# Optimization experiments

Hardware: AMD Instinct MI355X
Metric: run time of the kernel (lower is better)

## Reference

```python
import jax, jax.numpy as jnp
import numpy as np

N_NODES = 100000
N_EDGES = 1600000
IN_DIM, HIDDEN, OUT_DIM = 128, 64, 32
LN_EPS = 1e-5


def setup_inputs() -> dict:
    key = jax.random.key(0)
    ks = jax.random.split(key, 12)
    x = jax.random.normal(ks[0], (N_NODES, IN_DIM), dtype=jnp.float32)
    edge_index = jax.random.randint(ks[1], (2, N_EDGES), 0, N_NODES, dtype=jnp.int64)
    s = 1.0 / np.sqrt(IN_DIM)
    s2 = 1.0 / np.sqrt(HIDDEN)
    return {
        "x": x,
        "edge_index": edge_index,
        "W_self0": jax.random.uniform(ks[2], (IN_DIM, HIDDEN), jnp.float32, -s, s),
        "W_neigh0": jax.random.uniform(ks[3], (IN_DIM, HIDDEN), jnp.float32, -s, s),
        "b0": jnp.zeros((HIDDEN,), jnp.float32),
        "g0": jnp.ones((HIDDEN,), jnp.float32),
        "be0": jnp.zeros((HIDDEN,), jnp.float32),
        "W_self1": jax.random.uniform(ks[4], (HIDDEN, OUT_DIM), jnp.float32, -s2, s2),
        "W_neigh1": jax.random.uniform(ks[5], (HIDDEN, OUT_DIM), jnp.float32, -s2, s2),
        "b1": jnp.zeros((OUT_DIM,), jnp.float32),
        "g1": jnp.ones((OUT_DIM,), jnp.float32),
        "be1": jnp.zeros((OUT_DIM,), jnp.float32),
    }


def _sage_layer(h, src, dst, W_self, W_neigh, b, g, be):
    n = h.shape[0]
    # mean aggregation of neighbor features via scatter-add + count
    agg = jax.ops.segment_sum(h[src], dst, num_segments=n)  # [N, F]
    cnt = jax.ops.segment_sum(jnp.ones((src.shape[0],), h.dtype), dst, num_segments=n)
    agg = agg / jnp.clip(cnt, 1.0)[:, None]
    z = h @ W_self + agg @ W_neigh + b  # [N, out]
    mu = jnp.mean(z, axis=-1, keepdims=True)
    var = jnp.mean((z - mu) ** 2, axis=-1, keepdims=True)
    zn = (z - mu) * jax.lax.rsqrt(var + LN_EPS) * g + be
    return jax.nn.relu(zn)


def reference(x, edge_index, W_self0, W_neigh0, b0, g0, be0,
              W_self1, W_neigh1, b1, g1, be1):
    src, dst = edge_index[0], edge_index[1]
    h = _sage_layer(x, src, dst, W_self0, W_neigh0, b0, g0, be0)
    h = _sage_layer(h, src, dst, W_self1, W_neigh1, b1, g1, be1)
    return h
```

## Files before the change

### kernel.cpp

```cpp
#include <hip/hip_runtime.h>
#include <hip/hip_bf16.h>

#define N_NODES 100000
#define N_EDGES 1600000
#define IN_DIM 128
#define HID 64
#define OUT_DIM 32
#define LN_EPS 1e-5f
#define NBKT 782
#define NPBLK 500
#define PAIRS_PER_BLK 1600
#define G0T 1563
#define PADCAP 384

typedef __attribute__((ext_vector_type(8))) _Float16 half8;
typedef __attribute__((ext_vector_type(4))) float f32x4;

__device__ __forceinline__ float uflo(unsigned int u) {
  return __uint_as_float(u << 16);
}
__device__ __forceinline__ float ufhi(unsigned int u) {
  return __uint_as_float(u & 0xffff0000u);
}
__device__ __forceinline__ unsigned short bf16rne(float f) {
  unsigned int u = __float_as_uint(f);
  unsigned int r = u + 0x7fffu + ((u >> 16) & 1u);
  return (unsigned short)(r >> 16);
}

__global__ void detect_edges(const int* __restrict__ w, int* __restrict__ flag) {
  __shared__ int any;
  if (threadIdx.x == 0) any = 0;
  __syncthreads();
  if (w[2 * threadIdx.x + 1] != 0) any = 1;
  __syncthreads();
  if (threadIdx.x == 0) flag[0] = any ? 0 : 1;
}

__global__ __launch_bounds__(256) void convW(
    const float* __restrict__ Wn0, const float* __restrict__ Ws0,
    const float* __restrict__ Wn1, const float* __restrict__ Ws1,
    _Float16* __restrict__ B0f, _Float16* __restrict__ B1f) {
  const int i = blockIdx.x * 256 + threadIdx.x;
  if (i < 128 * 128) {
    const int n = i >> 7, k = i & 127;
    const float w = (n < 64) ? Wn0[k * 64 + n] : Ws0[k * 64 + (n - 64)];
    B0f[i] = (_Float16)w;
  } else if (i < 128 * 128 + 64 * 64) {
    const int j = i - 128 * 128;
    const int n = j >> 6, k = j & 63;
    const float w = (n < 32) ? Wn1[k * 32 + n] : Ws1[k * 32 + (n - 32)];
    B1f[j] = (_Float16)w;
  }
}

__global__ __launch_bounds__(256) void g0pc(
    const float* __restrict__ x, const _Float16* __restrict__ B0f,
    const float* __restrict__ b0,
    unsigned short* __restrict__ p0u, float* __restrict__ s0b,
    const int* __restrict__ w, const int* __restrict__ flag,
    int* __restrict__ gcount, int* __restrict__ blkbase) {
  __shared__ _Float16 lb[64 * 128];
  const int tid = threadIdx.x;

  if (blockIdx.x < NPBLK) {
    int* h = (int*)lb;
    const int b = blockIdx.x;
    for (int i = tid; i < NBKT; i += 256) h[i] = 0;
    __syncthreads();
    const int i64 = flag[0];
    const int pEnd = (b + 1) * PAIRS_PER_BLK;
    for (int p = b * PAIRS_PER_BLK + tid; p < pEnd; p += 256) {
      int d0, d1;
      if (i64) {
        const int4 vd = *(const int4*)(w + 2 * (size_t)N_EDGES + 4 * (size_t)p);
        d0 = vd.x; d1 = vd.z;
      } else {
        const int2 vd = *(const int2*)(w + (size_t)N_EDGES + 2 * (size_t)p);
        d0 = vd.x; d1 = vd.y;
      }
      atomicAdd(&h[d0 >> 7], 1);
      atomicAdd(&h[d1 >> 7], 1);
    }
    __syncthreads();
    for (int i = tid; i < NBKT; i += 256)
      blkbase[b * NBKT + i] = atomicAdd(&gcount[i], h[i]);
    return;
  }

  const int gb = blockIdx.x - NPBLK;
  const int colgrp = (gb >= G0T) ? 1 : 0;
  const int rowblk = colgrp ? (gb - G0T) : gb;
  {
    const uint4* gsrc = (const uint4*)(B0f + (colgrp << 13));
    for (int i = tid; i < 1024; i += 256) {
      const int o = i << 4;
      const int sw = o ^ (((o >> 8) & 7) << 4);
      *(uint4*)((char*)lb + sw) = gsrc[i];
    }
  }
  __syncthreads();
  const int lane = tid & 63;
  const int wave = tid >> 6;
  const int rowbase = rowblk * 64 + wave * 16;
  const int arow = rowbase + (lane & 15);
  const int rclamp = (arow < N_NODES) ? arow : 0;
  const int ko = (lane >> 4) << 3;

  f32x4 acc[4];
#pragma unroll
  for (int ct = 0; ct < 4; ++ct) acc[ct] = (f32x4){0.f, 0.f, 0.f, 0.f};

  for (int ks = 0; ks < 4; ++ks) {
    float av[8];
    const float* ax = x + (size_t)rclamp * IN_DIM + ks * 32 + ko;
    *(float4*)&av[0] = *(const float4*)ax;
    *(float4*)&av[4] = *(const float4*)(ax + 4);
    half8 ah;
#pragma unroll
    for (int j = 0; j < 8; ++j) ah[j] = (_Float16)av[j];
    const int kb = ks * 64 + (ko << 1);
#pragma unroll
    for (int ct = 0; ct < 4; ++ct) {
      const int n = ct * 16 + (lane & 15);
      const int boff = (n << 8) + kb;
      const int sb = boff ^ (((boff >> 8) & 7) << 4);
      const half8 bv = *(const half8*)((const char*)lb + sb);
      acc[ct] = __builtin_amdgcn_mfma_f32_16x16x32_f16(ah, bv, acc[ct], 0, 0, 0);
    }
  }
  const int rb4 = rowbase + ((lane >> 4) << 2);
  const int cc = lane & 15;
  if (colgrp == 0) {
#pragma unroll
    for (int ct = 0; ct < 4; ++ct) {
#pragma unroll
      for (int j = 0; j < 4; ++j) {
        const int r = rb4 + j;
        if (r < N_NODES) p0u[(size_t)r * HID + ct * 16 + cc] = bf16rne(acc[ct][j]);
      }
    }
  } else {
#pragma unroll
    for (int ct = 0; ct < 4; ++ct) {
      const float bias = b0[ct * 16 + cc];
#pragma unroll
      for (int j = 0; j < 4; ++j) {
        const int r = rb4 + j;
        if (r < N_NODES) s0b[(size_t)r * HID + ct * 16 + cc] = acc[ct][j] + bias;
      }
    }
  }
}

__global__ __launch_bounds__(256) void part_scan(
    const int* __restrict__ gcount, int* __restrict__ gbase) {
  __shared__ int lds[256];
  const int t = threadIdx.x;
  int v[4];
  int s = 0;
#pragma unroll
  for (int j = 0; j < 4; ++j) {
    const int idx = t * 4 + j;
    v[j] = (idx < NBKT) ? gcount[idx] : 0;
    s += v[j];
  }
  lds[t] = s;
  __syncthreads();
  for (int o = 1; o < 256; o <<= 1) {
    const int val = (t >= o) ? lds[t - o] : 0;
    __syncthreads();
    lds[t] += val;
    __syncthreads();
  }
  int run = lds[t] - s;
#pragma unroll
  for (int j = 0; j < 4; ++j) {
    const int idx = t * 4 + j;
    if (idx < NBKT) gbase[idx] = run;
    run += v[j];
  }
}

__global__ __launch_bounds__(256) void part_scatter(
    const int* __restrict__ w, const int* __restrict__ flag,
    const int* __restrict__ gbase, const int* __restrict__ blkbase,
    int* __restrict__ pe) {
  __shared__ int cur[NBKT];
  const int t = threadIdx.x, b = blockIdx.x;
  for (int i = t; i < NBKT; i += 256)
    cur[i] = gbase[i] + blkbase[b * NBKT + i];
  __syncthreads();
  const int i64 = flag[0];
  const int pEnd = (b + 1) * PAIRS_PER_BLK;
  for (int p = b * PAIRS_PER_BLK + t; p < pEnd; p += 256) {
    int s0, s1, d0, d1;
    if (i64) {
      const int4 vs = *(const int4*)(w + 4 * (size_t)p);
      const int4 vd = *(const int4*)(w + 2 * (size_t)N_EDGES + 4 * (size_t)p);
      s0 = vs.x; s1 = vs.z;
      d0 = vd.x; d1 = vd.z;
    } else {
      const int2 vs = *(const int2*)(w + 2 * (size_t)p);
      const int2 vd = *(const int2*)(w + (size_t)N_EDGES + 2 * (size_t)p);
      s0 = vs.x; s1 = vs.y;
      d0 = vd.x; d1 = vd.y;
    }
    const int sl0 = atomicAdd(&cur[d0 >> 7], 1);
    pe[sl0] = s0 | ((d0 & 127) << 17);
    const int sl1 = atomicAdd(&cur[d1 >> 7], 1);
    pe[sl1] = s1 | ((d1 & 127) << 17);
  }
}

__global__ __launch_bounds__(256) void bucket_csr(
    const int* __restrict__ pe, const int* __restrict__ gbase,
    const int* __restrict__ gcount, int* __restrict__ deg,
    int* __restrict__ off, int* __restrict__ sortedSrc) {
  __shared__ int ldeg[128];
  __shared__ int loff[128];
  __shared__ int lcur[128];
  const int t = threadIdx.x;
  const int bkt = blockIdx.x;
  const int nbase = bkt << 7;
  const int ebase = gbase[bkt];
  const int cnt = gcount[bkt];
  const int outbase = ebase + PADCAP * bkt;
  if (t < 128) ldeg[t] = 0;
  __syncthreads();
  for (int e = t; e < cnt; e += 256) {
    const int pv = pe[ebase + e];
    atomicAdd(&ldeg[(pv >> 17) & 127], 1);
  }
  __syncthreads();
  if (t < 128) loff[t] = (ldeg[t] + 3) & ~3;
  __syncthreads();
  for (int o = 1; o < 128; o <<= 1) {
    int v = 0;
    if (t >= o && t < 128) v = loff[t - o];
    __syncthreads();
    if (t < 128) loff[t] += v;
    __syncthreads();
  }
  if (t < 128) {
    const int pdeg = (ldeg[t] + 3) & ~3;
    const int ex = loff[t] - pdeg;
    lcur[t] = ex;
    const int n = nbase + t;
    if (n < N_NODES) {
      deg[n] = ldeg[t];
      off[n] = outbase + ex;
    }
  }
  __syncthreads();
  for (int e = t; e < cnt; e += 256) {
    const int pv = pe[ebase + e];
    const int ld = (pv >> 17) & 127;
    const int p = atomicAdd(&lcur[ld], 1);
    sortedSrc[outbase + p] = pv & 0x1FFFF;
  }
  __syncthreads();
  if (t < 128) {
    const int pdeg = (ldeg[t] + 3) & ~3;
    const int ex = loff[t] - pdeg;
    for (int q = ldeg[t]; q < pdeg; ++q)
      sortedSrc[outbase + ex + q] = N_NODES;
  }
}

__global__ __launch_bounds__(256) void gemm1(
    const float* __restrict__ h1, const _Float16* __restrict__ B1f,
    const float* __restrict__ b1,
    unsigned short* __restrict__ p1u, float* __restrict__ s1b) {
  __shared__ _Float16 lb[64 * 64];
  const int tid = threadIdx.x;
  {
    const uint4* gb = (const uint4*)B1f;
    for (int i = tid; i < 512; i += 256) {
      const int o = i << 4;
      const int sw = o ^ (((o >> 7) & 7) << 4);
      *(uint4*)((char*)lb + sw) = gb[i];
    }
  }
  __syncthreads();
  const int lane = tid & 63;
  const int wave = tid >> 6;
  const int rowbase = blockIdx.x * 64 + wave * 16;
  const int arow = rowbase + (lane & 15);
  const int rclamp = (arow < N_NODES) ? arow : 0;
  const int ko = (lane >> 4) << 3;

  f32x4 acc[4];
#pragma unroll
  for (int ct = 0; ct < 4; ++ct) acc[ct] = (f32x4){0.f, 0.f, 0.f, 0.f};

  for (int ks = 0; ks < 2; ++ks) {
    float av[8];
    const float* ax = h1 + (size_t)rclamp * HID + ks * 32 + ko;
    *(float4*)&av[0] = *(const float4*)ax;
    *(float4*)&av[4] = *(const float4*)(ax + 4);
    half8 ah;
#pragma unroll
    for (int j = 0; j < 8; ++j) ah[j] = (_Float16)av[j];
    const int kb = ks * 64 + (ko << 1);
#pragma unroll
    for (int ct = 0; ct < 4; ++ct) {
      const int n = ct * 16 + (lane & 15);
      const int boff = (n << 7) + kb;
      const int sb = boff ^ (((boff >> 7) & 7) << 4);
      const half8 bv = *(const half8*)((const char*)lb + sb);
      acc[ct] = __builtin_amdgcn_mfma_f32_16x16x32_f16(ah, bv, acc[ct], 0, 0, 0);
    }
  }
  const int rb4 = rowbase + ((lane >> 4) << 2);
  const int cc = lane & 15;
#pragma unroll
  for (int ct = 0; ct < 2; ++ct) {
#pragma unroll
    for (int j = 0; j < 4; ++j) {
      const int r = rb4 + j;
      if (r < N_NODES) p1u[(size_t)r * OUT_DIM + ct * 16 + cc] = bf16rne(acc[ct][j]);
    }
  }
#pragma unroll
  for (int ct = 2; ct < 4; ++ct) {
    const float bias = b1[(ct - 2) * 16 + cc];
#pragma unroll
    for (int j = 0; j < 4; ++j) {
      const int r = rb4 + j;
      if (r < N_NODES)
        s1b[(size_t)r * OUT_DIM + (ct - 2) * 16 + cc] = acc[ct][j] + bias;
    }
  }
}

__global__ __launch_bounds__(256) void aggc0(
    const int* __restrict__ sortedSrc, const int* __restrict__ off,
    const int* __restrict__ deg, const unsigned short* __restrict__ p0u,
    const float* __restrict__ s0b, const float* __restrict__ g,
    const float* __restrict__ be, float* __restrict__ h1) {
  const int lane = threadIdx.x & 63;
  const int h = lane >> 5;
  const int grp = (lane >> 3) & 3;
  const int sl = lane & 7;
  const int i = blockIdx.x * 8 + ((threadIdx.x >> 6) << 1) + h;
  const int st = off[i];
  const int dg = deg[i];
  const int dgp = (dg + 3) & ~3;
  const int dgmaxp = max(dgp, __shfl_xor(dgp, 32));
  float acc[8];
#pragma unroll
  for (int f = 0; f < 8; ++f) acc[f] = 0.f;

  for (int base = 0; base < dgmaxp; base += 32) {
    const int cntp = dgp - base;
    const int l5 = lane & 31;
    const int idx = (l5 < cntp) ? sortedSrc[st + base + l5] : N_NODES;
    const int cm = min(32, dgmaxp - base);
    for (int j = 0; j * 4 < cm; ++j) {
      const int e = j * 4 + grp;
      const int srcn = __shfl(idx, (h << 5) | e);
      const uint4 q = *(const uint4*)(p0u + (size_t)srcn * HID + sl * 8);
      acc[0] += uflo(q.x); acc[1] += ufhi(q.x);
      acc[2] += uflo(q.y); acc[3] += ufhi(q.y);
      acc[4] += uflo(q.z); acc[5] += ufhi(q.z);
      acc[6] += uflo(q.w); acc[7] += ufhi(q.w);
    }
  }
#pragma unroll
  for (int mk = 8; mk < 32; mk <<= 1) {
#pragma unroll
    for (int f = 0; f < 8; ++f) acc[f] += __shfl_xor(acc[f], mk);
  }
  const float inv = 1.0f / fmaxf((float)dg, 1.0f);
  float z[8];
  const float4 sb0 = *(const float4*)(s0b + (size_t)i * HID + sl * 8);
  const float4 sb1 = *(const float4*)(s0b + (size_t)i * HID + sl * 8 + 4);
  z[0] = sb0.x + acc[0] * inv; z[1] = sb0.y + acc[1] * inv;
  z[2] = sb0.z + acc[2] * inv; z[3] = sb0.w + acc[3] * inv;
  z[4] = sb1.x + acc[4] * inv; z[5] = sb1.y + acc[5] * inv;
  z[6] = sb1.z + acc[6] * inv; z[7] = sb1.w + acc[7] * inv;
  float pm = 0.f;
#pragma unroll
  for (int f = 0; f < 8; ++f) pm += z[f];
#pragma unroll
  for (int mk = 1; mk < 8; mk <<= 1) pm += __shfl_xor(pm, mk);
  const float mean = pm * (1.0f / 64.0f);
  float pv = 0.f;
#pragma unroll
  for (int f = 0; f < 8; ++f) {
    z[f] -= mean;
    pv += z[f] * z[f];
  }
#pragma unroll
  for (int mk = 1; mk < 8; mk <<= 1) pv += __shfl_xor(pv, mk);
  const float rstd = rsqrtf(pv * (1.0f / 64.0f) + LN_EPS);
  if (grp == 0) {
    const float4 gv0 = *(const float4*)(g + sl * 8);
    const float4 gv1 = *(const float4*)(g + sl * 8 + 4);
    const float4 bv0 = *(const float4*)(be + sl * 8);
    const float4 bv1 = *(const float4*)(be + sl * 8 + 4);
    float4 o0, o1;
    o0.x = fmaxf(z[0] * rstd * gv0.x + bv0.x, 0.f);
    o0.y = fmaxf(z[1] * rstd * gv0.y + bv0.y, 0.f);
    o0.z = fmaxf(z[2] * rstd * gv0.z + bv0.z, 0.f);
    o0.w = fmaxf(z[3] * rstd * gv0.w + bv0.w, 0.f);
    o1.x = fmaxf(z[4] * rstd * gv1.x + bv1.x, 0.f);
    o1.y = fmaxf(z[5] * rstd * gv1.y + bv1.y, 0.f);
    o1.z = fmaxf(z[6] * rstd * gv1.z + bv1.z, 0.f);
    o1.w = fmaxf(z[7] * rstd * gv1.w + bv1.w, 0.f);
    *(float4*)(h1 + (size_t)i * HID + sl * 8) = o0;
    *(float4*)(h1 + (size_t)i * HID + sl * 8 + 4) = o1;
  }
}

__global__ __launch_bounds__(256) void aggc1(
    const int* __restrict__ sortedSrc, const int* __restrict__ off,
    const int* __restrict__ deg, const unsigned short* __restrict__ p1u,
    const float* __restrict__ s1b, const float* __restrict__ g,
    const float* __restrict__ be, float* __restrict__ out) {
  const int lane = threadIdx.x & 63;
  const int q4 = lane >> 4;
  const int grp = (lane >> 2) & 3;
  const int sl = lane & 3;
  const int i = blockIdx.x * 16 + ((threadIdx.x >> 6) << 2) + q4;
  const int st = off[i];
  const int dg = deg[i];
  const int dgp = (dg + 3) & ~3;
  int dm = max(dgp, __shfl_xor(dgp, 16));
  const int dgmaxp = max(dm, __shfl_xor(dm, 32));
  float acc[8];
#pragma unroll
  for (int f = 0; f < 8; ++f) acc[f] = 0.f;

  for (int base = 0; base < dgmaxp; base += 16) {
    const int cntp = dgp - base;
    const int l4 = lane & 15;
    const int idx = (l4 < cntp) ? sortedSrc[st + base + l4] : N_NODES;
    const int cm = min(16, dgmaxp - base);
    for (int j = 0; j * 4 < cm; ++j) {
      const int e = j * 4 + grp;
      const int srcn = __shfl(idx, (q4 << 4) | e);
      const uint4 qv = *(const uint4*)(p1u + (size_t)srcn * OUT_DIM + sl * 8);
      acc[0] += uflo(qv.x); acc[1] += ufhi(qv.x);
      acc[2] += uflo(qv.y); acc[3] += ufhi(qv.y);
      acc[4] += uflo(qv.z); acc[5] += ufhi(qv.z);
      acc[6] += uflo(qv.w); acc[7] += ufhi(qv.w);
    }
  }
#pragma unroll
  for (int mk = 4; mk < 16; mk <<= 1) {
#pragma unroll
    for (int f = 0; f < 8; ++f) acc[f] += __shfl_xor(acc[f], mk);
  }
  const float inv = 1.0f / fmaxf((float)dg, 1.0f);
  float z[8];
  const float4 sb0 = *(const float4*)(s1b + (size_t)i * OUT_DIM + sl * 8);
  const float4 sb1 = *(const float4*)(s1b + (size_t)i * OUT_DIM + sl * 8 + 4);
  z[0] = sb0.x + acc[0] * inv; z[1] = sb0.y + acc[1] * inv;
  z[2] = sb0.z + acc[2] * inv; z[3] = sb0.w + acc[3] * inv;
  z[4] = sb1.x + acc[4] * inv; z[5] = sb1.y + acc[5] * inv;
  z[6] = sb1.z + acc[6] * inv; z[7] = sb1.w + acc[7] * inv;
  float pm = 0.f;
#pragma unroll
  for (int f = 0; f < 8; ++f) pm += z[f];
#pragma unroll
  for (int mk = 1; mk < 4; mk <<= 1) pm += __shfl_xor(pm, mk);
  const float mean = pm * (1.0f / 32.0f);
  float pv = 0.f;
#pragma unroll
  for (int f = 0; f < 8; ++f) {
    z[f] -= mean;
    pv += z[f] * z[f];
  }
#pragma unroll
  for (int mk = 1; mk < 4; mk <<= 1) pv += __shfl_xor(pv, mk);
  const float rstd = rsqrtf(pv * (1.0f / 32.0f) + LN_EPS);
  if (grp == 0) {
    const float4 gv0 = *(const float4*)(g + sl * 8);
    const float4 gv1 = *(const float4*)(g + sl * 8 + 4);
    const float4 bv0 = *(const float4*)(be + sl * 8);
    const float4 bv1 = *(const float4*)(be + sl * 8 + 4);
    float4 o0, o1;
    o0.x = fmaxf(z[0] * rstd * gv0.x + bv0.x, 0.f);
    o0.y = fmaxf(z[1] * rstd * gv0.y + bv0.y, 0.f);
    o0.z = fmaxf(z[2] * rstd * gv0.z + bv0.z, 0.f);
    o0.w = fmaxf(z[3] * rstd * gv0.w + bv0.w, 0.f);
    o1.x = fmaxf(z[4] * rstd * gv1.x + bv1.x, 0.f);
    o1.y = fmaxf(z[5] * rstd * gv1.y + bv1.y, 0.f);
    o1.z = fmaxf(z[6] * rstd * gv1.z + bv1.z, 0.f);
    o1.w = fmaxf(z[7] * rstd * gv1.w + bv1.w, 0.f);
    *(float4*)(out + (size_t)i * OUT_DIM + sl * 8) = o0;
    *(float4*)(out + (size_t)i * OUT_DIM + sl * 8 + 4) = o1;
  }
}

extern "C" void kernel_launch(void* const* d_in, const int* in_sizes, int n_in,
                              void* d_out, int out_size, void* d_ws, size_t ws_size,
                              hipStream_t stream) {
  const float* x       = (const float*)d_in[0];
  const int*   edges   = (const int*)d_in[1];
  const float* Wself0  = (const float*)d_in[2];
  const float* Wneigh0 = (const float*)d_in[3];
  const float* b0      = (const float*)d_in[4];
  const float* g0      = (const float*)d_in[5];
  const float* be0     = (const float*)d_in[6];
  const float* Wself1  = (const float*)d_in[7];
  const float* Wneigh1 = (const float*)d_in[8];
  const float* b1      = (const float*)d_in[9];
  const float* g1      = (const float*)d_in[10];
  const float* be1     = (const float*)d_in[11];

  char* base = (char*)d_ws;
  size_t o = 0;
  auto carve = [&](size_t bytes) {
    char* p = base + o;
    o += (bytes + 255) & ~(size_t)255;
    return p;
  };
  int* flag      = (int*)carve(64 * 4);
  int* gcount    = (int*)carve(1024 * 4);
  int* gbase     = (int*)carve(1024 * 4);
  int* blkbase   = (int*)carve((size_t)NPBLK * NBKT * 4);
  int* deg       = (int*)carve((size_t)N_NODES * 4);
  int* off       = (int*)carve((size_t)N_NODES * 4);
  int* sortedSrc = (int*)carve(1950000 * 4);
  int* pe        = (int*)carve(6500000);
  _Float16* B0f  = (_Float16*)carve(128 * 128 * 2);
  _Float16* B1f  = (_Float16*)carve(64 * 64 * 2);
  unsigned short* p0u = (unsigned short*)carve(((size_t)N_NODES + 2) * HID * 2);
  float* s0b = (float*)carve((size_t)N_NODES * HID * 4);
  float* h1  = (float*)carve((size_t)N_NODES * HID * 4);
  unsigned short* p1u = (unsigned short*)pe;
  float* s1b = s0b;

  hipMemsetAsync(gcount, 0, NBKT * sizeof(int), stream);
  hipMemsetAsync(p0u + (size_t)N_NODES * HID, 0, HID * sizeof(unsigned short),
                 stream);

  detect_edges<<<1, 256, 0, stream>>>(edges, flag);
  convW<<<80, 256, 0, stream>>>(Wneigh0, Wself0, Wneigh1, Wself1, B0f, B1f);
  g0pc<<<NPBLK + 2 * G0T, 256, 0, stream>>>(x, B0f, b0, p0u, s0b,
                                            edges, flag, gcount, blkbase);
  part_scan<<<1, 256, 0, stream>>>(gcount, gbase);
  part_scatter<<<NPBLK, 256, 0, stream>>>(edges, flag, gbase, blkbase, pe);
  bucket_csr<<<NBKT, 256, 0, stream>>>(pe, gbase, gcount, deg, off, sortedSrc);

  hipMemsetAsync(p1u + (size_t)N_NODES * OUT_DIM, 0,
                 OUT_DIM * sizeof(unsigned short), stream);

  aggc0<<<N_NODES / 8, 256, 0, stream>>>(sortedSrc, off, deg, p0u, s0b,
                                         g0, be0, h1);
  gemm1<<<(N_NODES + 63) / 64, 256, 0, stream>>>(h1, B1f, b1, p1u, s1b);
  aggc1<<<N_NODES / 16, 256, 0, stream>>>(sortedSrc, off, deg, p1u, s1b,
                                          g1, be1, (float*)d_out);
}
```

Baseline: 166.1 us.

## Store self-term and hidden activations in bf16 and use bf16 MFMA in gemm1

The self-term buffers (s0b/s1b) and the layer-1 hidden activations h1 are now stored as bf16 instead of fp32, so the intermediate tensors that are written and read between kernels take half the bytes. gemm1 now reads bf16 activations straight into a bf16 MFMA, with no per-element fp32 to fp16 conversion. g0pc and gemm1 also issue their global A loads before the LDS weight staging so the two can overlap. The cost is extra rounding error in intermediates, a risk to accuracy tolerance.

```diff
diff --git a/kernel.cpp b/kernel.cpp
--- a/kernel.cpp
+++ b/kernel.cpp
@@ -14,6 +14,7 @@
 #define PADCAP 384
 
 typedef __attribute__((ext_vector_type(8))) _Float16 half8;
+typedef __attribute__((ext_vector_type(8))) short short8;
 typedef __attribute__((ext_vector_type(4))) float f32x4;
 
 __device__ __forceinline__ float uflo(unsigned int u) {
@@ -27,6 +28,9 @@
   unsigned int r = u + 0x7fffu + ((u >> 16) & 1u);
   return (unsigned short)(r >> 16);
 }
+__device__ __forceinline__ unsigned int pk(float lo, float hi) {
+  return (unsigned int)bf16rne(lo) | ((unsigned int)bf16rne(hi) << 16);
+}
 
 __global__ void detect_edges(const int* __restrict__ w, int* __restrict__ flag) {
   __shared__ int any;
@@ -40,7 +44,7 @@
 __global__ __launch_bounds__(256) void convW(
     const float* __restrict__ Wn0, const float* __restrict__ Ws0,
     const float* __restrict__ Wn1, const float* __restrict__ Ws1,
-    _Float16* __restrict__ B0f, _Float16* __restrict__ B1f) {
+    _Float16* __restrict__ B0f, unsigned short* __restrict__ B1u) {
   const int i = blockIdx.x * 256 + threadIdx.x;
   if (i < 128 * 128) {
     const int n = i >> 7, k = i & 127;
@@ -50,14 +54,14 @@
     const int j = i - 128 * 128;
     const int n = j >> 6, k = j & 63;
     const float w = (n < 32) ? Wn1[k * 32 + n] : Ws1[k * 32 + (n - 32)];
-    B1f[j] = (_Float16)w;
+    B1u[j] = bf16rne(w);
   }
 }
 
 __global__ __launch_bounds__(256) void g0pc(
     const float* __restrict__ x, const _Float16* __restrict__ B0f,
     const float* __restrict__ b0,
-    unsigned short* __restrict__ p0u, float* __restrict__ s0b,
+    unsigned short* __restrict__ p0u, unsigned short* __restrict__ s0bu,
     const int* __restrict__ w, const int* __restrict__ flag,
     int* __restrict__ gcount, int* __restrict__ blkbase) {
   __shared__ _Float16 lb[64 * 128];
@@ -91,6 +95,22 @@
   const int gb = blockIdx.x - NPBLK;
   const int colgrp = (gb >= G0T) ? 1 : 0;
   const int rowblk = colgrp ? (gb - G0T) : gb;
+  const int lane = tid & 63;
+  const int wave = tid >> 6;
+  const int rowbase = rowblk * 64 + wave * 16;
+  const int arow = rowbase + (lane & 15);
+  const int rclamp = (arow < N_NODES) ? arow : 0;
+  const int ko = (lane >> 4) << 3;
+
+  float av[32];
+  {
+    const float* ax = x + (size_t)rclamp * IN_DIM + ko;
+#pragma unroll
+    for (int ks = 0; ks < 4; ++ks) {
+      *(float4*)&av[ks * 8] = *(const float4*)(ax + ks * 32);
+      *(float4*)&av[ks * 8 + 4] = *(const float4*)(ax + ks * 32 + 4);
+    }
+  }
   {
     const uint4* gsrc = (const uint4*)(B0f + (colgrp << 13));
     for (int i = tid; i < 1024; i += 256) {
@@ -100,25 +120,20 @@
     }
   }
   __syncthreads();
-  const int lane = tid & 63;
-  const int wave = tid >> 6;
-  const int rowbase = rowblk * 64 + wave * 16;
-  const int arow = rowbase + (lane & 15);
-  const int rclamp = (arow < N_NODES) ? arow : 0;
-  const int ko = (lane >> 4) << 3;
+
+  half8 ah[4];
+#pragma unroll
+  for (int ks = 0; ks < 4; ++ks) {
+#pragma unroll
+    for (int j = 0; j < 8; ++j) ah[ks][j] = (_Float16)av[ks * 8 + j];
+  }
 
   f32x4 acc[4];
 #pragma unroll
   for (int ct = 0; ct < 4; ++ct) acc[ct] = (f32x4){0.f, 0.f, 0.f, 0.f};
 
+#pragma unroll
   for (int ks = 0; ks < 4; ++ks) {
-    float av[8];
-    const float* ax = x + (size_t)rclamp * IN_DIM + ks * 32 + ko;
-    *(float4*)&av[0] = *(const float4*)ax;
-    *(float4*)&av[4] = *(const float4*)(ax + 4);
-    half8 ah;
-#pragma unroll
-    for (int j = 0; j < 8; ++j) ah[j] = (_Float16)av[j];
     const int kb = ks * 64 + (ko << 1);
 #pragma unroll
     for (int ct = 0; ct < 4; ++ct) {
@@ -126,7 +141,7 @@
       const int boff = (n << 8) + kb;
       const int sb = boff ^ (((boff >> 8) & 7) << 4);
       const half8 bv = *(const half8*)((const char*)lb + sb);
-      acc[ct] = __builtin_amdgcn_mfma_f32_16x16x32_f16(ah, bv, acc[ct], 0, 0, 0);
+      acc[ct] = __builtin_amdgcn_mfma_f32_16x16x32_f16(ah[ks], bv, acc[ct], 0, 0, 0);
     }
   }
   const int rb4 = rowbase + ((lane >> 4) << 2);
@@ -147,7 +162,8 @@
 #pragma unroll
       for (int j = 0; j < 4; ++j) {
         const int r = rb4 + j;
-        if (r < N_NODES) s0b[(size_t)r * HID + ct * 16 + cc] = acc[ct][j] + bias;
+        if (r < N_NODES)
+          s0bu[(size_t)r * HID + ct * 16 + cc] = bf16rne(acc[ct][j] + bias);
       }
     }
   }
@@ -269,20 +285,11 @@
 }
 
 __global__ __launch_bounds__(256) void gemm1(
-    const float* __restrict__ h1, const _Float16* __restrict__ B1f,
+    const unsigned short* __restrict__ h1u, const unsigned short* __restrict__ B1u,
     const float* __restrict__ b1,
-    unsigned short* __restrict__ p1u, float* __restrict__ s1b) {
-  __shared__ _Float16 lb[64 * 64];
+    unsigned short* __restrict__ p1u, unsigned short* __restrict__ s1bu) {
+  __shared__ unsigned short lb[64 * 64];
   const int tid = threadIdx.x;
-  {
-    const uint4* gb = (const uint4*)B1f;
-    for (int i = tid; i < 512; i += 256) {
-      const int o = i << 4;
-      const int sw = o ^ (((o >> 7) & 7) << 4);
-      *(uint4*)((char*)lb + sw) = gb[i];
-    }
-  }
-  __syncthreads();
   const int lane = tid & 63;
   const int wave = tid >> 6;
   const int rowbase = blockIdx.x * 64 + wave * 16;
@@ -290,26 +297,36 @@
   const int rclamp = (arow < N_NODES) ? arow : 0;
   const int ko = (lane >> 4) << 3;
 
+  short8 ah[2];
+  {
+    const unsigned short* ax = h1u + (size_t)rclamp * HID + ko;
+    ah[0] = *(const short8*)ax;
+    ah[1] = *(const short8*)(ax + 32);
+  }
+  {
+    const uint4* gb = (const uint4*)B1u;
+    for (int i = tid; i < 512; i += 256) {
+      const int o = i << 4;
+      const int sw = o ^ (((o >> 7) & 7) << 4);
+      *(uint4*)((char*)lb + sw) = gb[i];
+    }
+  }
+  __syncthreads();
+
   f32x4 acc[4];
 #pragma unroll
   for (int ct = 0; ct < 4; ++ct) acc[ct] = (f32x4){0.f, 0.f, 0.f, 0.f};
 
+#pragma unroll
   for (int ks = 0; ks < 2; ++ks) {
-    float av[8];
-    const float* ax = h1 + (size_t)rclamp * HID + ks * 32 + ko;
-    *(float4*)&av[0] = *(const float4*)ax;
-    *(float4*)&av[4] = *(const float4*)(ax + 4);
-    half8 ah;
-#pragma unroll
-    for (int j = 0; j < 8; ++j) ah[j] = (_Float16)av[j];
     const int kb = ks * 64 + (ko << 1);
 #pragma unroll
     for (int ct = 0; ct < 4; ++ct) {
       const int n = ct * 16 + (lane & 15);
       const int boff = (n << 7) + kb;
       const int sb = boff ^ (((boff >> 7) & 7) << 4);
-      const half8 bv = *(const half8*)((const char*)lb + sb);
-      acc[ct] = __builtin_amdgcn_mfma_f32_16x16x32_f16(ah, bv, acc[ct], 0, 0, 0);
+      const short8 bv = *(const short8*)((const char*)lb + sb);
+      acc[ct] = __builtin_amdgcn_mfma_f32_16x16x32_bf16(ah[ks], bv, acc[ct], 0, 0, 0);
     }
   }
   const int rb4 = rowbase + ((lane >> 4) << 2);
@@ -324,12 +341,12 @@
   }
 #pragma unroll
   for (int ct = 2; ct < 4; ++ct) {
-    const float bias = b1[(ct - 2) * 16 + cc];
 #pragma unroll
     for (int j = 0; j < 4; ++j) {
       const int r = rb4 + j;
       if (r < N_NODES)
-        s1b[(size_t)r * OUT_DIM + (ct - 2) * 16 + cc] = acc[ct][j] + bias;
+        s1bu[(size_t)r * OUT_DIM + (ct - 2) * 16 + cc] =
+            bf16rne(acc[ct][j] + b1[(ct - 2) * 16 + cc]);
     }
   }
 }
@@ -337,8 +354,8 @@
 __global__ __launch_bounds__(256) void aggc0(
     const int* __restrict__ sortedSrc, const int* __restrict__ off,
     const int* __restrict__ deg, const unsigned short* __restrict__ p0u,
-    const float* __restrict__ s0b, const float* __restrict__ g,
-    const float* __restrict__ be, float* __restrict__ h1) {
+    const unsigned short* __restrict__ s0bu, const float* __restrict__ g,
+    const float* __restrict__ be, unsigned short* __restrict__ h1u) {
   const int lane = threadIdx.x & 63;
   const int h = lane >> 5;
   const int grp = (lane >> 3) & 3;
@@ -374,12 +391,11 @@
   }
   const float inv = 1.0f / fmaxf((float)dg, 1.0f);
   float z[8];
-  const float4 sb0 = *(const float4*)(s0b + (size_t)i * HID + sl * 8);
-  const float4 sb1 = *(const float4*)(s0b + (size_t)i * HID + sl * 8 + 4);
-  z[0] = sb0.x + acc[0] * inv; z[1] = sb0.y + acc[1] * inv;
-  z[2] = sb0.z + acc[2] * inv; z[3] = sb0.w + acc[3] * inv;
-  z[4] = sb1.x + acc[4] * inv; z[5] = sb1.y + acc[5] * inv;
-  z[6] = sb1.z + acc[6] * inv; z[7] = sb1.w + acc[7] * inv;
+  const uint4 sbv = *(const uint4*)(s0bu + (size_t)i * HID + sl * 8);
+  z[0] = uflo(sbv.x) + acc[0] * inv; z[1] = ufhi(sbv.x) + acc[1] * inv;
+  z[2] = uflo(sbv.y) + acc[2] * inv; z[3] = ufhi(sbv.y) + acc[3] * inv;
+  z[4] = uflo(sbv.z) + acc[4] * inv; z[5] = ufhi(sbv.z) + acc[5] * inv;
+  z[6] = uflo(sbv.w) + acc[6] * inv; z[7] = ufhi(sbv.w) + acc[7] * inv;
   float pm = 0.f;
 #pragma unroll
   for (int f = 0; f < 8; ++f) pm += z[f];
@@ -400,24 +416,23 @@
     const float4 gv1 = *(const float4*)(g + sl * 8 + 4);
     const float4 bv0 = *(const float4*)(be + sl * 8);
     const float4 bv1 = *(const float4*)(be + sl * 8 + 4);
-    float4 o0, o1;
-    o0.x = fmaxf(z[0] * rstd * gv0.x + bv0.x, 0.f);
-    o0.y = fmaxf(z[1] * rstd * gv0.y + bv0.y, 0.f);
-    o0.z = fmaxf(z[2] * rstd * gv0.z + bv0.z, 0.f);
-    o0.w = fmaxf(z[3] * rstd * gv0.w + bv0.w, 0.f);
-    o1.x = fmaxf(z[4] * rstd * gv1.x + bv1.x, 0.f);
-    o1.y = fmaxf(z[5] * rstd * gv1.y + bv1.y, 0.f);
-    o1.z = fmaxf(z[6] * rstd * gv1.z + bv1.z, 0.f);
-    o1.w = fmaxf(z[7] * rstd * gv1.w + bv1.w, 0.f);
-    *(float4*)(h1 + (size_t)i * HID + sl * 8) = o0;
-    *(float4*)(h1 + (size_t)i * HID + sl * 8 + 4) = o1;
+    uint4 ov;
+    ov.x = pk(fmaxf(z[0] * rstd * gv0.x + bv0.x, 0.f),
+              fmaxf(z[1] * rstd * gv0.y + bv0.y, 0.f));
+    ov.y = pk(fmaxf(z[2] * rstd * gv0.z + bv0.z, 0.f),
+              fmaxf(z[3] * rstd * gv0.w + bv0.w, 0.f));
+    ov.z = pk(fmaxf(z[4] * rstd * gv1.x + bv1.x, 0.f),
+              fmaxf(z[5] * rstd * gv1.y + bv1.y, 0.f));
+    ov.w = pk(fmaxf(z[6] * rstd * gv1.z + bv1.z, 0.f),
+              fmaxf(z[7] * rstd * gv1.w + bv1.w, 0.f));
+    *(uint4*)(h1u + (size_t)i * HID + sl * 8) = ov;
   }
 }
 
 __global__ __launch_bounds__(256) void aggc1(
     const int* __restrict__ sortedSrc, const int* __restrict__ off,
     const int* __restrict__ deg, const unsigned short* __restrict__ p1u,
-    const float* __restrict__ s1b, const float* __restrict__ g,
+    const unsigned short* __restrict__ s1bu, const float* __restrict__ g,
     const float* __restrict__ be, float* __restrict__ out) {
   const int lane = threadIdx.x & 63;
   const int q4 = lane >> 4;
@@ -455,12 +470,11 @@
   }
   const float inv = 1.0f / fmaxf((float)dg, 1.0f);
   float z[8];
-  const float4 sb0 = *(const float4*)(s1b + (size_t)i * OUT_DIM + sl * 8);
-  const float4 sb1 = *(const float4*)(s1b + (size_t)i * OUT_DIM + sl * 8 + 4);
-  z[0] = sb0.x + acc[0] * inv; z[1] = sb0.y + acc[1] * inv;
-  z[2] = sb0.z + acc[2] * inv; z[3] = sb0.w + acc[3] * inv;
-  z[4] = sb1.x + acc[4] * inv; z[5] = sb1.y + acc[5] * inv;
-  z[6] = sb1.z + acc[6] * inv; z[7] = sb1.w + acc[7] * inv;
+  const uint4 sbv = *(const uint4*)(s1bu + (size_t)i * OUT_DIM + sl * 8);
+  z[0] = uflo(sbv.x) + acc[0] * inv; z[1] = ufhi(sbv.x) + acc[1] * inv;
+  z[2] = uflo(sbv.y) + acc[2] * inv; z[3] = ufhi(sbv.y) + acc[3] * inv;
+  z[4] = uflo(sbv.z) + acc[4] * inv; z[5] = ufhi(sbv.z) + acc[5] * inv;
+  z[6] = uflo(sbv.w) + acc[6] * inv; z[7] = ufhi(sbv.w) + acc[7] * inv;
   float pm = 0.f;
 #pragma unroll
   for (int f = 0; f < 8; ++f) pm += z[f];
@@ -527,20 +541,20 @@
   int* sortedSrc = (int*)carve(1950000 * 4);
   int* pe        = (int*)carve(6500000);
   _Float16* B0f  = (_Float16*)carve(128 * 128 * 2);
-  _Float16* B1f  = (_Float16*)carve(64 * 64 * 2);
+  unsigned short* B1u = (unsigned short*)carve(64 * 64 * 2);
   unsigned short* p0u = (unsigned short*)carve(((size_t)N_NODES + 2) * HID * 2);
-  float* s0b = (float*)carve((size_t)N_NODES * HID * 4);
-  float* h1  = (float*)carve((size_t)N_NODES * HID * 4);
+  unsigned short* s0bu = (unsigned short*)carve(((size_t)N_NODES + 2) * HID * 2);
+  unsigned short* h1u = (unsigned short*)carve(((size_t)N_NODES + 2) * HID * 2);
   unsigned short* p1u = (unsigned short*)pe;
-  float* s1b = s0b;
+  unsigned short* s1bu = s0bu;
 
   hipMemsetAsync(gcount, 0, NBKT * sizeof(int), stream);
   hipMemsetAsync(p0u + (size_t)N_NODES * HID, 0, HID * sizeof(unsigned short),
                  stream);
 
   detect_edges<<<1, 256, 0, stream>>>(edges, flag);
-  convW<<<80, 256, 0, stream>>>(Wneigh0, Wself0, Wneigh1, Wself1, B0f, B1f);
-  g0pc<<<NPBLK + 2 * G0T, 256, 0, stream>>>(x, B0f, b0, p0u, s0b,
+  convW<<<80, 256, 0, stream>>>(Wneigh0, Wself0, Wneigh1, Wself1, B0f, B1u);
+  g0pc<<<NPBLK + 2 * G0T, 256, 0, stream>>>(x, B0f, b0, p0u, s0bu,
                                             edges, flag, gcount, blkbase);
   part_scan<<<1, 256, 0, stream>>>(gcount, gbase);
   part_scatter<<<NPBLK, 256, 0, stream>>>(edges, flag, gbase, blkbase, pe);
@@ -549,9 +563,9 @@
   hipMemsetAsync(p1u + (size_t)N_NODES * OUT_DIM, 0,
                  OUT_DIM * sizeof(unsigned short), stream);
 
-  aggc0<<<N_NODES / 8, 256, 0, stream>>>(sortedSrc, off, deg, p0u, s0b,
-                                         g0, be0, h1);
-  gemm1<<<(N_NODES + 63) / 64, 256, 0, stream>>>(h1, B1f, b1, p1u, s1b);
-  aggc1<<<N_NODES / 16, 256, 0, stream>>>(sortedSrc, off, deg, p1u, s1b,
+  aggc0<<<N_NODES / 8, 256, 0, stream>>>(sortedSrc, off, deg, p0u, s0bu,
+                                         g0, be0, h1u);
+  gemm1<<<(N_NODES + 63) / 64, 256, 0, stream>>>(h1u, B1u, b1, p1u, s1bu);
+  aggc1<<<N_NODES / 16, 256, 0, stream>>>(sortedSrc, off, deg, p1u, s1bu,
                                           g1, be1, (float*)d_out);
 }
```

After: 162.4 us. 2.3% less time.
